# Kernel optimization log

Measured on AMD Instinct MI355X. Metric: run time of the kernel, lower is better.

The kernel has to match this reference:

```python
import jax, jax.numpy as jnp
import numpy as np

HIDDEN = 3072
NUM_HEADS = 24
HEAD_DIM = HIDDEN // NUM_HEADS  # 128
MLP_HIDDEN = 4 * HIDDEN         # 12288
SEQ = 2048


def setup_inputs() -> dict:
    key = jax.random.key(0)
    ks = jax.random.split(key, 12)
    s = 0.02
    return {
        "x": jax.random.normal(ks[0], (1, SEQ, HIDDEN), jnp.float32),
        "vec": jax.random.normal(ks[1], (1, HIDDEN), jnp.float32),
        "pe": jax.random.normal(ks[2], (1, 1, SEQ, HEAD_DIM // 2, 2, 2), jnp.float32),
        "mod_w": jax.random.normal(ks[3], (HIDDEN, 3 * HIDDEN), jnp.float32) * s,
        "mod_b": jnp.zeros((3 * HIDDEN,), jnp.float32),
        "lin1_w": jax.random.normal(ks[4], (HIDDEN, 3 * HIDDEN + MLP_HIDDEN), jnp.float32) * s,
        "lin1_b": jnp.zeros((3 * HIDDEN + MLP_HIDDEN,), jnp.float32),
        "lin2_w": jax.random.normal(ks[5], (HIDDEN + MLP_HIDDEN, HIDDEN), jnp.float32) * s,
        "lin2_b": jnp.zeros((HIDDEN,), jnp.float32),
        "q_scale": jnp.ones((HEAD_DIM,), jnp.float32),
        "k_scale": jnp.ones((HEAD_DIM,), jnp.float32),
    }


def _forward(x, vec, pe, mod_w, mod_b, lin1_w, lin1_b, lin2_w, lin2_b, q_scale, k_scale):
    B, L, H = x.shape
    NH, HD = NUM_HEADS, HEAD_DIM

    # Modulation: lin(silu(vec)) -> shift, scale, gate  (flux Modulation, double=False)
    mod = jnp.dot(jax.nn.silu(vec), mod_w) + mod_b          # (B, 3H)
    shift, scale, gate = jnp.split(mod, 3, axis=-1)
    shift, scale, gate = shift[:, None, :], scale[:, None, :], gate[:, None, :]

    # LayerNorm (no affine, eps=1e-6) + scale/shift modulation
    mu = jnp.mean(x, axis=-1, keepdims=True)
    var = jnp.mean((x - mu) ** 2, axis=-1, keepdims=True)
    xn = (x - mu) * jax.lax.rsqrt(var + 1e-6)
    x_mod = (1.0 + scale) * xn + shift

    # Fused QKV + MLP projection
    h = jnp.dot(x_mod, lin1_w) + lin1_b                     # (B, L, 3H + MLP)
    qkv, mlp = h[..., : 3 * H], h[..., 3 * H :]
    qkv = qkv.reshape(B, L, 3, NH, HD).transpose(2, 0, 3, 1, 4)  # (3, B, NH, L, HD)
    q, k, v = qkv[0], qkv[1], qkv[2]

    # QKNorm: RMSNorm over head_dim with learned scale (eps=1e-6)
    def rms(t, s):
        return t * jax.lax.rsqrt(jnp.mean(t * t, axis=-1, keepdims=True) + 1e-6) * s

    q = rms(q, q_scale)
    k = rms(k, k_scale)

    # Rotary embedding: pe is (B, 1, L, HD/2, 2, 2) of rotation matrix rows
    def rope(t):
        tr = t.reshape(B, NH, L, HD // 2, 1, 2)
        out = pe[..., 0] * tr[..., 0] + pe[..., 1] * tr[..., 1]  # (B, NH, L, HD/2, 2)
        return out.reshape(B, NH, L, HD)

    q, k = rope(q), rope(k)

    # Scaled dot-product attention (default 1/sqrt(HD) scale)
    scores = jnp.einsum("bhqd,bhkd->bhqk", q, k) / jnp.sqrt(jnp.float32(HD))
    attn = jnp.einsum("bhqk,bhkd->bhqd", jax.nn.softmax(scores, axis=-1), v)
    attn = attn.transpose(0, 2, 1, 3).reshape(B, L, H)

    # GELU(tanh) MLP branch, concat, output projection, gated residual
    mlp_act = jax.nn.gelu(mlp, approximate=True)
    out = jnp.dot(jnp.concatenate([attn, mlp_act], axis=-1), lin2_w) + lin2_b
    return x + gate * out


def reference(x, vec, pe, mod_w, mod_b, lin1_w, lin1_b, lin2_w, lin2_b, q_scale, k_scale):
    return _forward(x, vec, pe, mod_w, mod_b, lin1_w, lin1_b, lin2_w, lin2_b, q_scale, k_scale)
```

## Files before the change

kernel.cpp:

```cpp
#include <hip/hip_runtime.h>
#include <hip/hip_bf16.h>
#include <stdint.h>

#define SEQ   2048
#define HID   3072
#define NHEADS 24
#define HDIM  128
#define MLPD  12288
#define NCOL1 21504
#define NCOL2 15360
#define MOD3  9216
#define QKVW  9216
#define KSPLIT 8

typedef __attribute__((ext_vector_type(4))) float f32x4;
typedef __attribute__((ext_vector_type(8))) short bf16x8;
typedef __attribute__((ext_vector_type(4))) unsigned short u16x4;
typedef __attribute__((ext_vector_type(2))) unsigned short u16x2;

#define VMC(n) asm volatile("s_waitcnt vmcnt(" #n ")" ::: "memory")
#define SB()   __builtin_amdgcn_sched_barrier(0)

__device__ __forceinline__ unsigned short f2bf(float f){
  unsigned u = __float_as_uint(f);
  u = (u + 0x7fffu + ((u >> 16) & 1u)) >> 16;
  return (unsigned short)u;
}
__device__ __forceinline__ float bf2f(unsigned short u){
  return __uint_as_float(((unsigned)u) << 16);
}

__device__ __forceinline__ void gload_lds16(const void* g, void* l){
  __builtin_amdgcn_global_load_lds(
      (const __attribute__((address_space(1))) unsigned int*)g,
      (__attribute__((address_space(3))) unsigned int*)l, 16, 0, 0);
}

__device__ __forceinline__ float gelu_tanh(float x){
  float u = 0.7978845608028654f * (x + 0.044715f * x * x * x);
  float t = 1.f - 2.f / (__expf(2.f * u) + 1.f);
  return 0.5f * x * (1.f + t);
}

__global__ void silu_kernel(const float* __restrict__ vec, float* __restrict__ sv){
  int i = blockIdx.x * 256 + threadIdx.x;
  if (i < HID){ float v = vec[i]; sv[i] = v / (1.f + __expf(-v)); }
}

__global__ void mod_gemv(const float* __restrict__ sv, const float* __restrict__ W,
                         const float* __restrict__ b, float* __restrict__ mod){
  int n  = blockIdx.x * 32 + (threadIdx.x & 31);
  int ks = threadIdx.x >> 5;
  float acc = 0.f;
  int k0 = ks * 384;
  #pragma unroll 4
  for (int k = k0; k < k0 + 384; ++k)
    acc += sv[k] * W[(size_t)k * MOD3 + n];
  __shared__ float red[8][32];
  red[ks][threadIdx.x & 31] = acc;
  __syncthreads();
  if (ks == 0){
    float a = 0.f;
    #pragma unroll
    for (int i = 0; i < 8; ++i) a += red[i][threadIdx.x & 31];
    mod[n] = a + b[n];
  }
}

__global__ __launch_bounds__(256)
void ln_mod_kernel(const float* __restrict__ x, const float* __restrict__ mod,
                   unsigned short* __restrict__ xmod){
  int l = blockIdx.x, t = threadIdx.x;
  const float* row = x + (size_t)l * HID;
  f32x4 v[3];
  float s = 0.f, s2 = 0.f;
  #pragma unroll
  for (int i = 0; i < 3; ++i){
    v[i] = *(const f32x4*)(row + (t + i * 256) * 4);
    #pragma unroll
    for (int j = 0; j < 4; ++j){ s += v[i][j]; s2 += v[i][j] * v[i][j]; }
  }
  #pragma unroll
  for (int m = 1; m < 64; m <<= 1){ s += __shfl_xor(s, m, 64); s2 += __shfl_xor(s2, m, 64); }
  __shared__ float red[8];
  int wv = t >> 6, ln = t & 63;
  if (ln == 0){ red[wv] = s; red[4 + wv] = s2; }
  __syncthreads();
  s  = red[0] + red[1] + red[2] + red[3];
  s2 = red[4] + red[5] + red[6] + red[7];
  float mu  = s * (1.f / HID);
  float var = s2 * (1.f / HID) - mu * mu;
  float rs  = rsqrtf(var + 1e-6f);
  #pragma unroll
  for (int i = 0; i < 3; ++i){
    int c = (t + i * 256) * 4;
    f32x4 sh = *(const f32x4*)(mod + c);
    f32x4 sc = *(const f32x4*)(mod + HID + c);
    u16x4 o;
    #pragma unroll
    for (int j = 0; j < 4; ++j){
      float xn = (v[i][j] - mu) * rs;
      o[j] = f2bf((1.f + sc[j]) * xn + sh[j]);
    }
    *(u16x4*)(xmod + (size_t)l * HID + c) = o;
  }
}

__global__ __launch_bounds__(256)
void transpose_f2b(const float* __restrict__ in, unsigned short* __restrict__ out,
                   int R, int C){
  __shared__ float tile[64][65];
  int rt = blockIdx.y * 64, ct = blockIdx.x * 64;
  int t = threadIdx.x;
  int r0 = t >> 4, c0 = (t & 15) * 4;
  #pragma unroll
  for (int ph = 0; ph < 4; ++ph){
    int r = r0 + ph * 16;
    f32x4 v = *(const f32x4*)(in + (size_t)(rt + r) * C + ct + c0);
    tile[r][c0 + 0] = v[0]; tile[r][c0 + 1] = v[1];
    tile[r][c0 + 2] = v[2]; tile[r][c0 + 3] = v[3];
  }
  __syncthreads();
  #pragma unroll
  for (int ph = 0; ph < 4; ++ph){
    int r = r0 + ph * 16;
    u16x4 o;
    #pragma unroll
    for (int i = 0; i < 4; ++i) o[i] = f2bf(tile[c0 + i][r]);
    *(u16x4*)(out + (size_t)(ct + r) * R + rt + c0) = o;
  }
}

__global__ __launch_bounds__(256)
void transpose_b2b_head(const unsigned short* __restrict__ in,
                        unsigned short* __restrict__ out, int R, int C){
  __shared__ unsigned short tile[64][68];
  int h = blockIdx.z;
  const unsigned short* inh = in + (size_t)h * R * C;
  unsigned short* outh = out + (size_t)h * R * C;
  int rt = blockIdx.y * 64, ct = blockIdx.x * 64;
  int t = threadIdx.x;
  int r0 = t >> 4, c0 = (t & 15) * 4;
  #pragma unroll
  for (int ph = 0; ph < 4; ++ph){
    int r = r0 + ph * 16;
    u16x4 v = *(const u16x4*)(inh + (size_t)(rt + r) * C + ct + c0);
    tile[r][c0 + 0] = v[0]; tile[r][c0 + 1] = v[1];
    tile[r][c0 + 2] = v[2]; tile[r][c0 + 3] = v[3];
  }
  __syncthreads();
  #pragma unroll
  for (int ph = 0; ph < 4; ++ph){
    int r = r0 + ph * 16;
    u16x4 o;
    #pragma unroll
    for (int i = 0; i < 4; ++i) o[i] = tile[c0 + i][r];
    *(u16x4*)(outh + (size_t)(ct + r) * R + rt + c0) = o;
  }
}

__global__ void qkv_prep(const unsigned short* __restrict__ hq, const float* __restrict__ pe,
                         const float* __restrict__ qscale, const float* __restrict__ kscale,
                         unsigned short* __restrict__ qb, unsigned short* __restrict__ kb,
                         unsigned short* __restrict__ vb){
  int l = blockIdx.x, hh = blockIdx.y, lane = threadIdx.x;
  const unsigned short* row = hq + (size_t)l * QKVW;
  int d = lane * 2;
  u16x2 qv = *(const u16x2*)(row + hh * HDIM + d);
  u16x2 kv = *(const u16x2*)(row + HID + hh * HDIM + d);
  u16x2 vv = *(const u16x2*)(row + 2 * HID + hh * HDIM + d);
  float qx = bf2f(qv[0]), qy = bf2f(qv[1]);
  float kx = bf2f(kv[0]), ky = bf2f(kv[1]);
  float sq = qx * qx + qy * qy;
  float sk = kx * kx + ky * ky;
  #pragma unroll
  for (int m = 1; m < 64; m <<= 1){ sq += __shfl_xor(sq, m, 64); sk += __shfl_xor(sk, m, 64); }
  float rq = rsqrtf(sq * (1.f / HDIM) + 1e-6f);
  float rk = rsqrtf(sk * (1.f / HDIM) + 1e-6f);
  float2 qs2 = *(const float2*)(qscale + d);
  float2 ks2 = *(const float2*)(kscale + d);
  float q0 = qx * rq * qs2.x, q1 = qy * rq * qs2.y;
  float k0 = kx * rk * ks2.x, k1 = ky * rk * ks2.y;
  f32x4 p4 = *(const f32x4*)(pe + (size_t)l * 256 + lane * 4);
  const float sscl = 0.08838834764831845f;
  float qo0 = (p4[0] * q0 + p4[1] * q1) * sscl;
  float qo1 = (p4[2] * q0 + p4[3] * q1) * sscl;
  float ko0 =  p4[0] * k0 + p4[1] * k1;
  float ko1 =  p4[2] * k0 + p4[3] * k1;
  size_t base = ((size_t)hh * SEQ + l) * HDIM + d;
  u16x2 o;
  o[0] = f2bf(qo0); o[1] = f2bf(qo1); *(u16x2*)(qb + base) = o;
  o[0] = f2bf(ko0); o[1] = f2bf(ko1); *(u16x2*)(kb + base) = o;
  o[0] = vv[0];     o[1] = vv[1];     *(u16x2*)(vb + base) = o;
}

template<int EPI>
__global__ __launch_bounds__(512)
void gemm256(const unsigned short* __restrict__ A, const unsigned short* __restrict__ BT,
             const float* __restrict__ bias, unsigned short* __restrict__ out0,
             unsigned short* __restrict__ out1,
             int M, int N, int ldA, int ldB, int kchunk){
  __shared__ unsigned short Ls[65536];
  int nxy = gridDim.x * gridDim.y;
  int nwg = nxy * gridDim.z;
  int fid = (blockIdx.z * gridDim.y + blockIdx.y) * gridDim.x + blockIdx.x;
  int nid = (fid & 7) * (nwg >> 3) + (fid >> 3);
  int ksz = nid / nxy, rem = nid % nxy;
  int bm  = rem % gridDim.y, bn = rem / gridDim.y;
  int k0 = ksz * kchunk;
  int nk = kchunk >> 6;
  int tid = threadIdx.x, wave = tid >> 6, lane = tid & 63, lg = lane >> 4, lr = lane & 15;
  int wr = wave >> 2, wc = wave & 3;

  int G0 = tid, G1 = tid + 512;
  int r0 = G0 >> 2, r1 = G1 >> 2;
  int c0 = ((G0 & 3) ^ ((r0 >> 1) & 3)) * 8;
  int c1 = ((G1 & 3) ^ ((r1 >> 1) & 3)) * 8;
  const unsigned short* A0 = A  + (size_t)(bm * 256 + r0) * ldA + k0 + c0;
  const unsigned short* A1 = A  + (size_t)(bm * 256 + r1) * ldA + k0 + c1;
  const unsigned short* B0 = BT + (size_t)(bn * 256 + r0) * ldB + k0 + c0;
  const unsigned short* B1 = BT + (size_t)(bn * 256 + r1) * ldB + k0 + c1;
  unsigned short* LA = Ls;
  unsigned short* LB = Ls + 32768;
  int d0 = (wave * 64) * 8, d1 = (512 + wave * 64) * 8;

  auto stageA = [&](int t, int kh){
    unsigned short* h = LA + (((t & 1) * 2 + kh) << 13);
    int kc = t * 64 + kh * 32;
    gload_lds16(A0 + kc, h + d0);
    gload_lds16(A1 + kc, h + d1);
  };
  auto stageB = [&](int t, int kh){
    unsigned short* h = LB + (((t & 1) * 2 + kh) << 13);
    int kc = t * 64 + kh * 32;
    gload_lds16(B0 + kc, h + d0);
    gload_lds16(B1 + kc, h + d1);
  };

  int offA[8], offB[4];
  #pragma unroll
  for (int m = 0; m < 8; ++m){
    int row = wr * 128 + m * 16 + lr;
    offA[m] = row * 32 + ((lg ^ ((row >> 1) & 3)) * 8);
  }
  #pragma unroll
  for (int n = 0; n < 4; ++n){
    int row = wc * 64 + n * 16 + lr;
    offB[n] = row * 32 + ((lg ^ ((row >> 1) & 3)) * 8);
  }

  const f32x4 fz = 0.0f;
  f32x4 acc[8][4];
  #pragma unroll
  for (int i = 0; i < 8; ++i)
    #pragma unroll
    for (int j = 0; j < 4; ++j) acc[i][j] = fz;

  stageA(0, 0); stageB(0, 0); stageA(0, 1); stageB(0, 1); stageA(1, 0); stageB(1, 0);
  VMC(8);
  __builtin_amdgcn_s_barrier();
  SB();

  for (int t = 0; t < nk; ++t){
    const unsigned short* Ah = LA + (((t & 1) * 2) << 13);
    const unsigned short* Bh = LB + (((t & 1) * 2) << 13);
    bf16x8 fA[8], fB[4], gA[8], gB[4];
    #pragma unroll
    for (int m = 0; m < 4; ++m) fA[m] = *(const bf16x8*)&Ah[offA[m]];
    #pragma unroll
    for (int n = 0; n < 4; ++n) fB[n] = *(const bf16x8*)&Bh[offB[n]];
    #pragma unroll
    for (int m = 4; m < 8; ++m) fA[m] = *(const bf16x8*)&Ah[offA[m]];
    if (t + 1 < nk) stageA(t + 1, 1);
    SB();
    __builtin_amdgcn_s_barrier();
    SB();
    __builtin_amdgcn_s_setprio(1);
    #pragma unroll
    for (int m = 0; m < 4; ++m)
      #pragma unroll
      for (int n = 0; n < 4; ++n)
        acc[m][n] = __builtin_amdgcn_mfma_f32_16x16x32_bf16(fA[m], fB[n], acc[m][n], 0, 0, 0);
    __builtin_amdgcn_s_setprio(0);
    SB();
    __builtin_amdgcn_s_barrier();
    if (t + 1 < nk) stageB(t + 1, 1);
    SB();
    if (t == nk - 1) VMC(0);
    else             VMC(8);
    __builtin_amdgcn_s_barrier();
    SB();
    #pragma unroll
    for (int m = 0; m < 4; ++m) gA[m] = *(const bf16x8*)&Ah[8192 + offA[m]];
    #pragma unroll
    for (int n = 0; n < 4; ++n) gB[n] = *(const bf16x8*)&Bh[8192 + offB[n]];
    SB();
    __builtin_amdgcn_s_setprio(1);
    #pragma unroll
    for (int m = 0; m < 4; ++m)
      #pragma unroll
      for (int n = 0; n < 4; ++n)
        acc[m + 4][n] = __builtin_amdgcn_mfma_f32_16x16x32_bf16(fA[m + 4], fB[n], acc[m + 4][n], 0, 0, 0);
    __builtin_amdgcn_s_setprio(0);
    SB();
    __builtin_amdgcn_s_barrier();
    #pragma unroll
    for (int m = 4; m < 8; ++m) gA[m] = *(const bf16x8*)&Ah[8192 + offA[m]];
    if (t + 2 < nk) stageA(t + 2, 0);
    SB();
    __builtin_amdgcn_s_barrier();
    SB();
    __builtin_amdgcn_s_setprio(1);
    #pragma unroll
    for (int m = 0; m < 4; ++m)
      #pragma unroll
      for (int n = 0; n < 4; ++n)
        acc[m][n] = __builtin_amdgcn_mfma_f32_16x16x32_bf16(gA[m], gB[n], acc[m][n], 0, 0, 0);
    __builtin_amdgcn_s_setprio(0);
    SB();
    __builtin_amdgcn_s_barrier();
    if (t + 2 < nk) stageB(t + 2, 0);
    SB();
    if (t <= nk - 3)      VMC(8);
    else if (t == nk - 2) VMC(4);
    __builtin_amdgcn_s_barrier();
    SB();
    __builtin_amdgcn_s_setprio(1);
    #pragma unroll
    for (int m = 0; m < 4; ++m)
      #pragma unroll
      for (int n = 0; n < 4; ++n)
        acc[m + 4][n] = __builtin_amdgcn_mfma_f32_16x16x32_bf16(gA[m + 4], gB[n], acc[m + 4][n], 0, 0, 0);
    __builtin_amdgcn_s_setprio(0);
    SB();
    __builtin_amdgcn_s_barrier();
  }

  if constexpr (EPI == 0){
    if (bn < MOD3 / 256){
      #pragma unroll
      for (int m = 0; m < 8; ++m)
        #pragma unroll
        for (int n = 0; n < 4; ++n){
          int col = bn * 256 + wc * 64 + n * 16 + lr;
          float bv = bias[col];
          #pragma unroll
          for (int jj = 0; jj < 4; ++jj){
            int row = bm * 256 + wr * 128 + m * 16 + lg * 4 + jj;
            out0[(size_t)row * QKVW + col] = f2bf(acc[m][n][jj] + bv);
          }
        }
    } else {
      #pragma unroll
      for (int m = 0; m < 8; ++m)
        #pragma unroll
        for (int n = 0; n < 4; ++n){
          int col = bn * 256 + wc * 64 + n * 16 + lr;
          float bv = bias[col];
          #pragma unroll
          for (int jj = 0; jj < 4; ++jj){
            int row = bm * 256 + wr * 128 + m * 16 + lg * 4 + jj;
            out1[(size_t)row * NCOL2 + (col - 2 * HID)] = f2bf(gelu_tanh(acc[m][n][jj] + bv));
          }
        }
    }
  } else {
    unsigned short* P = out0 + (size_t)ksz * M * N;
    #pragma unroll
    for (int m = 0; m < 8; ++m)
      #pragma unroll
      for (int n = 0; n < 4; ++n){
        int col = bn * 256 + wc * 64 + n * 16 + lr;
        #pragma unroll
        for (int jj = 0; jj < 4; ++jj){
          int row = bm * 256 + wr * 128 + m * 16 + lg * 4 + jj;
          P[(size_t)row * N + col] = f2bf(acc[m][n][jj]);
        }
      }
  }
}

__global__ __launch_bounds__(256)
void reduce_lin2(const unsigned short* __restrict__ part, const float* __restrict__ x,
                 const float* __restrict__ gate, const float* __restrict__ bias,
                 float* __restrict__ out){
  int i4 = blockIdx.x * 256 + threadIdx.x;
  int c4 = i4 % (HID / 4);
  f32x4 s = 0.0f;
  #pragma unroll
  for (int ks = 0; ks < KSPLIT; ++ks){
    u16x4 p = *(const u16x4*)(part + (size_t)ks * SEQ * HID + (size_t)i4 * 4);
    #pragma unroll
    for (int j = 0; j < 4; ++j) s[j] += bf2f(p[j]);
  }
  f32x4 xv = *(const f32x4*)(x + (size_t)i4 * 4);
  f32x4 gv = *(const f32x4*)(gate + c4 * 4);
  f32x4 bv = *(const f32x4*)(bias + c4 * 4);
  f32x4 o;
  #pragma unroll
  for (int j = 0; j < 4; ++j) o[j] = xv[j] + gv[j] * (s[j] + bv[j]);
  *(f32x4*)(out + (size_t)i4 * 4) = o;
}

__global__ __launch_bounds__(256)
void attn_kernel(const unsigned short* __restrict__ qb, const unsigned short* __restrict__ kb,
                 const unsigned short* __restrict__ vt, unsigned short* __restrict__ a2){
  __shared__ unsigned short Ksm[64 * 128];
  __shared__ unsigned short Vsm[128 * 64];
  __shared__ unsigned short Psm[4][16 * 64];
  int fid = blockIdx.y * gridDim.x + blockIdx.x;
  int nid = (fid & 7) * 96 + (fid >> 3);
  int hh = nid / (SEQ / 64), qt = nid % (SEQ / 64);
  int tid = threadIdx.x, wave = tid >> 6, lane = tid & 63, lg = lane >> 4, lr = lane & 15;
  const unsigned short* Kh = kb + (size_t)hh * SEQ * HDIM;
  const unsigned short* Vh = vt + (size_t)hh * HDIM * SEQ;
  const unsigned short* Qh = qb + (size_t)hh * SEQ * HDIM;
  int q0 = qt * 64 + wave * 16;

  bf16x8 aq[4];
  #pragma unroll
  for (int kk = 0; kk < 4; ++kk)
    aq[kk] = *(const bf16x8*)(Qh + (size_t)(q0 + lr) * HDIM + kk * 32 + lg * 8);

  const f32x4 fzero = 0.0f;
  f32x4 acc_o[8];
  #pragma unroll
  for (int n = 0; n < 8; ++n) acc_o[n] = fzero;
  float mrun[4] = {-1e30f, -1e30f, -1e30f, -1e30f};
  float lrun[4] = {0.f, 0.f, 0.f, 0.f};

  for (int t = 0; t < SEQ / 64; ++t){
    __syncthreads();
    const unsigned short* Kt = Kh + (size_t)t * 64 * HDIM;
    const unsigned short* Vt = Vh + t * 64;
    #pragma unroll
    for (int r = 0; r < 4; ++r){
      int G  = r * 256 + tid;
      int Gs = G ^ ((G >> 4) & 7);
      gload_lds16(Kt + Gs * 8, (void*)&Ksm[(r * 256 + wave * 64) * 8]);
      int Gv = G ^ ((G >> 3) & 7);
      gload_lds16(Vt + (size_t)(Gv >> 3) * SEQ + (Gv & 7) * 8,
                  (void*)&Vsm[(r * 256 + wave * 64) * 8]);
    }
    __syncthreads();

    f32x4 sacc[4];
    #pragma unroll
    for (int j = 0; j < 4; ++j) sacc[j] = fzero;
    #pragma unroll
    for (int j = 0; j < 4; ++j){
      int kv = j * 16 + lr;
      #pragma unroll
      for (int kk = 0; kk < 4; ++kk){
        int bo = kv * 256 + (kk * 32 + lg * 8) * 2;
        bo ^= (kv & 7) << 4;
        bf16x8 bk = *(const bf16x8*)((const char*)Ksm + bo);
        sacc[j] = __builtin_amdgcn_mfma_f32_16x16x32_bf16(aq[kk], bk, sacc[j], 0, 0, 0);
      }
    }
    float scl[4], psum[4];
    #pragma unroll
    for (int jj = 0; jj < 4; ++jj){
      float m_ = fmaxf(fmaxf(sacc[0][jj], sacc[1][jj]), fmaxf(sacc[2][jj], sacc[3][jj]));
      #pragma unroll
      for (int mk = 1; mk < 16; mk <<= 1) m_ = fmaxf(m_, __shfl_xor(m_, mk, 64));
      float mn = fmaxf(mrun[jj], m_);
      scl[jj] = __expf(mrun[jj] - mn);
      mrun[jj] = mn;
      psum[jj] = 0.f;
    }
    #pragma unroll
    for (int j = 0; j < 4; ++j)
      #pragma unroll
      for (int jj = 0; jj < 4; ++jj){
        float p = __expf(sacc[j][jj] - mrun[jj]);
        sacc[j][jj] = p;
        psum[jj] += p;
      }
    #pragma unroll
    for (int jj = 0; jj < 4; ++jj){
      float ps = psum[jj];
      #pragma unroll
      for (int mk = 1; mk < 16; mk <<= 1) ps += __shfl_xor(ps, mk, 64);
      lrun[jj] = lrun[jj] * scl[jj] + ps;
    }
    #pragma unroll
    for (int n = 0; n < 8; ++n)
      #pragma unroll
      for (int jj = 0; jj < 4; ++jj) acc_o[n][jj] *= scl[jj];
    unsigned short* Pw = Psm[wave];
    #pragma unroll
    for (int j = 0; j < 4; ++j)
      #pragma unroll
      for (int jj = 0; jj < 4; ++jj){
        int prow = lg * 4 + jj, pcol = j * 16 + lr;
        int bo = prow * 128 + pcol * 2;
        bo ^= (prow & 7) << 4;
        *(unsigned short*)((char*)Pw + bo) = f2bf(sacc[j][jj]);
      }
    __syncthreads();
    #pragma unroll
    for (int k2 = 0; k2 < 2; ++k2){
      int bo = lr * 128 + (k2 * 32 + lg * 8) * 2;
      bo ^= (lr & 7) << 4;
      bf16x8 pf = *(const bf16x8*)((const char*)Pw + bo);
      #pragma unroll
      for (int n = 0; n < 8; ++n){
        int dd = n * 16 + lr;
        int vb_ = dd * 128 + (k2 * 32 + lg * 8) * 2;
        vb_ ^= (dd & 7) << 4;
        bf16x8 vf = *(const bf16x8*)((const char*)Vsm + vb_);
        acc_o[n] = __builtin_amdgcn_mfma_f32_16x16x32_bf16(pf, vf, acc_o[n], 0, 0, 0);
      }
    }
  }
  #pragma unroll
  for (int jj = 0; jj < 4; ++jj) lrun[jj] = 1.f / lrun[jj];
  #pragma unroll
  for (int n = 0; n < 8; ++n)
    #pragma unroll
    for (int jj = 0; jj < 4; ++jj){
      int row = q0 + lg * 4 + jj;
      int col = hh * HDIM + n * 16 + lr;
      a2[(size_t)row * NCOL2 + col] = f2bf(acc_o[n][jj] * lrun[jj]);
    }
}

extern "C" void kernel_launch(void* const* d_in, const int* in_sizes, int n_in,
                              void* d_out, int out_size, void* d_ws, size_t ws_size,
                              hipStream_t stream){
  const float* x       = (const float*)d_in[0];
  const float* vec     = (const float*)d_in[1];
  const float* pe      = (const float*)d_in[2];
  const float* mod_w   = (const float*)d_in[3];
  const float* mod_b   = (const float*)d_in[4];
  const float* lin1_w  = (const float*)d_in[5];
  const float* lin1_b  = (const float*)d_in[6];
  const float* lin2_w  = (const float*)d_in[7];
  const float* lin2_b  = (const float*)d_in[8];
  const float* q_scale = (const float*)d_in[9];
  const float* k_scale = (const float*)d_in[10];
  float* out = (float*)d_out;

  char* ws = (char*)d_ws;
  size_t off = 0;
  auto alloc = [&](size_t bytes){ void* p = ws + off; off += (bytes + 255) & ~(size_t)255; return p; };
  float* sv            = (float*)alloc((size_t)HID * 4);
  float* mod           = (float*)alloc((size_t)MOD3 * 4);
  unsigned short* xmod = (unsigned short*)alloc((size_t)SEQ * HID * 2);
  unsigned short* wt2  = (unsigned short*)alloc((size_t)HID * NCOL2 * 2);
  unsigned short* a2   = (unsigned short*)alloc((size_t)SEQ * NCOL2 * 2);
  unsigned short* qb   = (unsigned short*)alloc((size_t)NHEADS * SEQ * HDIM * 2);
  unsigned short* kb   = (unsigned short*)alloc((size_t)NHEADS * SEQ * HDIM * 2);
  unsigned short* vb   = (unsigned short*)alloc((size_t)NHEADS * SEQ * HDIM * 2);
  unsigned short* vt   = (unsigned short*)alloc((size_t)NHEADS * SEQ * HDIM * 2);
  unsigned short* wt1  = (unsigned short*)alloc((size_t)NCOL1 * HID * 2);
  unsigned short* hq   = (unsigned short*)alloc((size_t)SEQ * QKVW * 2);
  unsigned short* part = qb;

  silu_kernel<<<12, 256, 0, stream>>>(vec, sv);
  mod_gemv<<<MOD3 / 32, 256, 0, stream>>>(sv, mod_w, mod_b, mod);
  transpose_f2b<<<dim3(NCOL1 / 64, HID / 64), 256, 0, stream>>>(lin1_w, wt1, HID, NCOL1);
  transpose_f2b<<<dim3(HID / 64, NCOL2 / 64), 256, 0, stream>>>(lin2_w, wt2, NCOL2, HID);
  ln_mod_kernel<<<SEQ, 256, 0, stream>>>(x, mod, xmod);
  gemm256<0><<<dim3(NCOL1 / 256, SEQ / 256, 1), 512, 0, stream>>>(
      xmod, wt1, lin1_b, hq, a2, SEQ, NCOL1, HID, HID, HID);
  qkv_prep<<<dim3(SEQ, NHEADS), 64, 0, stream>>>(hq, pe, q_scale, k_scale, qb, kb, vb);
  transpose_b2b_head<<<dim3(HDIM / 64, SEQ / 64, NHEADS), 256, 0, stream>>>(vb, vt, SEQ, HDIM);
  attn_kernel<<<dim3(SEQ / 64, NHEADS), 256, 0, stream>>>(qb, kb, vt, a2);
  gemm256<2><<<dim3(HID / 256, SEQ / 256, KSPLIT), 512, 0, stream>>>(
      a2, wt2, nullptr, part, nullptr, SEQ, HID, NCOL2, NCOL2, NCOL2 / KSPLIT);
  reduce_lin2<<<SEQ * HID / 4 / 256, 256, 0, stream>>>(part, x, mod + 2 * HID, lin2_b, out);
}
```

Baseline: 834.7 us.

## Double-buffer K/V tiles in attention and fuse SiLU into modulation GEMV

Attention now keeps two LDS buffers for K and V and prefetches the next tile with async global-to-LDS loads while computing the current one, synchronized by vmcnt waits and raw barriers. The barrier after writing P is replaced by a per-wave LDS wait, since each wave only reads its own P. Separately, the SiLU of the modulation vector is computed inline in the GEMV, removing a kernel launch and a workspace buffer. The extra LDS doubles K/V shared memory usage, which may reduce occupancy.

```diff
diff --git a/kernel.cpp b/kernel.cpp
--- a/kernel.cpp
+++ b/kernel.cpp
@@ -42,20 +42,18 @@
   return 0.5f * x * (1.f + t);
 }
 
-__global__ void silu_kernel(const float* __restrict__ vec, float* __restrict__ sv){
-  int i = blockIdx.x * 256 + threadIdx.x;
-  if (i < HID){ float v = vec[i]; sv[i] = v / (1.f + __expf(-v)); }
-}
-
-__global__ void mod_gemv(const float* __restrict__ sv, const float* __restrict__ W,
+__global__ void mod_gemv(const float* __restrict__ vec, const float* __restrict__ W,
                          const float* __restrict__ b, float* __restrict__ mod){
   int n  = blockIdx.x * 32 + (threadIdx.x & 31);
   int ks = threadIdx.x >> 5;
   float acc = 0.f;
   int k0 = ks * 384;
   #pragma unroll 4
-  for (int k = k0; k < k0 + 384; ++k)
-    acc += sv[k] * W[(size_t)k * MOD3 + n];
+  for (int k = k0; k < k0 + 384; ++k){
+    float v = vec[k];
+    float s = v / (1.f + __expf(-v));
+    acc += s * W[(size_t)k * MOD3 + n];
+  }
   __shared__ float red[8][32];
   red[ks][threadIdx.x & 31] = acc;
   __syncthreads();
@@ -405,8 +403,8 @@
 __global__ __launch_bounds__(256)
 void attn_kernel(const unsigned short* __restrict__ qb, const unsigned short* __restrict__ kb,
                  const unsigned short* __restrict__ vt, unsigned short* __restrict__ a2){
-  __shared__ unsigned short Ksm[64 * 128];
-  __shared__ unsigned short Vsm[128 * 64];
+  __shared__ unsigned short Ksm[2][64 * 128];
+  __shared__ unsigned short Vsm[2][128 * 64];
   __shared__ unsigned short Psm[4][16 * 64];
   int fid = blockIdx.y * gridDim.x + blockIdx.x;
   int nid = (fid & 7) * 96 + (fid >> 3);
@@ -429,20 +427,28 @@
   float mrun[4] = {-1e30f, -1e30f, -1e30f, -1e30f};
   float lrun[4] = {0.f, 0.f, 0.f, 0.f};
 
-  for (int t = 0; t < SEQ / 64; ++t){
-    __syncthreads();
+  auto stage = [&](int t){
+    int buf = t & 1;
     const unsigned short* Kt = Kh + (size_t)t * 64 * HDIM;
     const unsigned short* Vt = Vh + t * 64;
     #pragma unroll
     for (int r = 0; r < 4; ++r){
       int G  = r * 256 + tid;
       int Gs = G ^ ((G >> 4) & 7);
-      gload_lds16(Kt + Gs * 8, (void*)&Ksm[(r * 256 + wave * 64) * 8]);
+      gload_lds16(Kt + Gs * 8, (void*)&Ksm[buf][(r * 256 + wave * 64) * 8]);
       int Gv = G ^ ((G >> 3) & 7);
       gload_lds16(Vt + (size_t)(Gv >> 3) * SEQ + (Gv & 7) * 8,
-                  (void*)&Vsm[(r * 256 + wave * 64) * 8]);
-    }
-    __syncthreads();
+                  (void*)&Vsm[buf][(r * 256 + wave * 64) * 8]);
+    }
+  };
+
+  stage(0);
+  for (int t = 0; t < SEQ / 64; ++t){
+    int buf = t & 1;
+    if (t + 1 < SEQ / 64){ stage(t + 1); VMC(8); }
+    else                 { VMC(0); }
+    __builtin_amdgcn_s_barrier();
+    SB();
 
     f32x4 sacc[4];
     #pragma unroll
@@ -454,7 +460,7 @@
       for (int kk = 0; kk < 4; ++kk){
         int bo = kv * 256 + (kk * 32 + lg * 8) * 2;
         bo ^= (kv & 7) << 4;
-        bf16x8 bk = *(const bf16x8*)((const char*)Ksm + bo);
+        bf16x8 bk = *(const bf16x8*)((const char*)Ksm[buf] + bo);
         sacc[j] = __builtin_amdgcn_mfma_f32_16x16x32_bf16(aq[kk], bk, sacc[j], 0, 0, 0);
       }
     }
@@ -498,7 +504,8 @@
         bo ^= (prow & 7) << 4;
         *(unsigned short*)((char*)Pw + bo) = f2bf(sacc[j][jj]);
       }
-    __syncthreads();
+    asm volatile("s_waitcnt lgkmcnt(0)" ::: "memory");
+    SB();
     #pragma unroll
     for (int k2 = 0; k2 < 2; ++k2){
       int bo = lr * 128 + (k2 * 32 + lg * 8) * 2;
@@ -509,10 +516,12 @@
         int dd = n * 16 + lr;
         int vb_ = dd * 128 + (k2 * 32 + lg * 8) * 2;
         vb_ ^= (dd & 7) << 4;
-        bf16x8 vf = *(const bf16x8*)((const char*)Vsm + vb_);
+        bf16x8 vf = *(const bf16x8*)((const char*)Vsm[buf] + vb_);
         acc_o[n] = __builtin_amdgcn_mfma_f32_16x16x32_bf16(pf, vf, acc_o[n], 0, 0, 0);
       }
     }
+    SB();
+    __builtin_amdgcn_s_barrier();
   }
   #pragma unroll
   for (int jj = 0; jj < 4; ++jj) lrun[jj] = 1.f / lrun[jj];
@@ -545,7 +554,6 @@
   char* ws = (char*)d_ws;
   size_t off = 0;
   auto alloc = [&](size_t bytes){ void* p = ws + off; off += (bytes + 255) & ~(size_t)255; return p; };
-  float* sv            = (float*)alloc((size_t)HID * 4);
   float* mod           = (float*)alloc((size_t)MOD3 * 4);
   unsigned short* xmod = (unsigned short*)alloc((size_t)SEQ * HID * 2);
   unsigned short* wt2  = (unsigned short*)alloc((size_t)HID * NCOL2 * 2);
@@ -558,8 +566,7 @@
   unsigned short* hq   = (unsigned short*)alloc((size_t)SEQ * QKVW * 2);
   unsigned short* part = qb;
 
-  silu_kernel<<<12, 256, 0, stream>>>(vec, sv);
-  mod_gemv<<<MOD3 / 32, 256, 0, stream>>>(sv, mod_w, mod_b, mod);
+  mod_gemv<<<MOD3 / 32, 256, 0, stream>>>(vec, mod_w, mod_b, mod);
   transpose_f2b<<<dim3(NCOL1 / 64, HID / 64), 256, 0, stream>>>(lin1_w, wt1, HID, NCOL1);
   transpose_f2b<<<dim3(HID / 64, NCOL2 / 64), 256, 0, stream>>>(lin2_w, wt2, NCOL2, HID);
   ln_mod_kernel<<<SEQ, 256, 0, stream>>>(x, mod, xmod);
```

New measurement: 841.8 us. About the same (+0.9%).

## Restructure GEMM staging into row-halves with full-K64 tiles and new wave mapping

Applied to the files above, without the earlier changes.

The 256x256 GEMM main loop now stages LDS by row halves (rows 0-127 and 128-255), each holding the full 64-wide K slice with an 8-way XOR swizzle, instead of splitting K into two 32-wide halves. Each wave now owns four 64x32 quadrant sub-tiles. It loads A and B fragments once per K step and reuses them across two K sub-steps, which cuts LDS reads and barriers per iteration. Wait counts and the epilogue row/column mapping are rewritten to match. This risks higher register pressure and subtle sync or waitcnt mistakes at the pipeline edges.

```diff
diff --git a/kernel.cpp b/kernel.cpp
--- a/kernel.cpp
+++ b/kernel.cpp
@@ -212,41 +212,41 @@
   int tid = threadIdx.x, wave = tid >> 6, lane = tid & 63, lg = lane >> 4, lr = lane & 15;
   int wr = wave >> 2, wc = wave & 3;
 
-  int G0 = tid, G1 = tid + 512;
-  int r0 = G0 >> 2, r1 = G1 >> 2;
-  int c0 = ((G0 & 3) ^ ((r0 >> 1) & 3)) * 8;
-  int c1 = ((G1 & 3) ^ ((r1 >> 1) & 3)) * 8;
-  const unsigned short* A0 = A  + (size_t)(bm * 256 + r0) * ldA + k0 + c0;
-  const unsigned short* A1 = A  + (size_t)(bm * 256 + r1) * ldA + k0 + c1;
-  const unsigned short* B0 = BT + (size_t)(bn * 256 + r0) * ldB + k0 + c0;
-  const unsigned short* B1 = BT + (size_t)(bn * 256 + r1) * ldB + k0 + c1;
-  unsigned short* LA = Ls;
-  unsigned short* LB = Ls + 32768;
+  int rh = tid >> 3;
+  int sc = (((tid & 7) ^ (rh & 7)) * 8);
+  const unsigned short* pA0 = A  + (size_t)(bm * 256 + rh     ) * ldA + k0 + sc;
+  const unsigned short* pA1 = A  + (size_t)(bm * 256 + rh + 64) * ldA + k0 + sc;
+  const unsigned short* pB0 = BT + (size_t)(bn * 256 + rh     ) * ldB + k0 + sc;
+  const unsigned short* pB1 = BT + (size_t)(bn * 256 + rh + 64) * ldB + k0 + sc;
   int d0 = (wave * 64) * 8, d1 = (512 + wave * 64) * 8;
 
-  auto stageA = [&](int t, int kh){
-    unsigned short* h = LA + (((t & 1) * 2 + kh) << 13);
-    int kc = t * 64 + kh * 32;
-    gload_lds16(A0 + kc, h + d0);
-    gload_lds16(A1 + kc, h + d1);
+  auto stageA = [&](int t, int half){
+    unsigned short* h = Ls + (((t & 1) * 2 + half) << 13);
+    size_t ro = (size_t)(half * 128) * ldA + t * 64;
+    gload_lds16(pA0 + ro, h + d0);
+    gload_lds16(pA1 + ro, h + d1);
   };
-  auto stageB = [&](int t, int kh){
-    unsigned short* h = LB + (((t & 1) * 2 + kh) << 13);
-    int kc = t * 64 + kh * 32;
-    gload_lds16(B0 + kc, h + d0);
-    gload_lds16(B1 + kc, h + d1);
+  auto stageB = [&](int t, int half){
+    unsigned short* h = Ls + 32768 + (((t & 1) * 2 + half) << 13);
+    size_t ro = (size_t)(half * 128) * ldB + t * 64;
+    gload_lds16(pB0 + ro, h + d0);
+    gload_lds16(pB1 + ro, h + d1);
   };
 
-  int offA[8], offB[4];
-  #pragma unroll
-  for (int m = 0; m < 8; ++m){
-    int row = wr * 128 + m * 16 + lr;
-    offA[m] = row * 32 + ((lg ^ ((row >> 1) & 3)) * 8);
-  }
-  #pragma unroll
-  for (int n = 0; n < 4; ++n){
-    int row = wc * 64 + n * 16 + lr;
-    offB[n] = row * 32 + ((lg ^ ((row >> 1) & 3)) * 8);
+  int offA[4][2], offB[2][2];
+  #pragma unroll
+  for (int mm = 0; mm < 4; ++mm){
+    int row = wr * 64 + mm * 16 + lr;
+    #pragma unroll
+    for (int ks = 0; ks < 2; ++ks)
+      offA[mm][ks] = row * 64 + (((ks * 4 + lg) ^ (row & 7)) * 8);
+  }
+  #pragma unroll
+  for (int nn = 0; nn < 2; ++nn){
+    int row = wc * 32 + nn * 16 + lr;
+    #pragma unroll
+    for (int ks = 0; ks < 2; ++ks)
+      offB[nn][ks] = row * 64 + (((ks * 4 + lg) ^ (row & 7)) * 8);
   }
 
   const f32x4 fz = 0.0f;
@@ -256,84 +256,91 @@
     #pragma unroll
     for (int j = 0; j < 4; ++j) acc[i][j] = fz;
 
-  stageA(0, 0); stageB(0, 0); stageA(0, 1); stageB(0, 1); stageA(1, 0); stageB(1, 0);
-  VMC(8);
-  __builtin_amdgcn_s_barrier();
-  SB();
+  stageA(0, 0); stageB(0, 0); stageB(0, 1); stageA(0, 1);
+  if (nk > 1){ stageA(1, 0); stageB(1, 0); }
 
   for (int t = 0; t < nk; ++t){
-    const unsigned short* Ah = LA + (((t & 1) * 2) << 13);
-    const unsigned short* Bh = LB + (((t & 1) * 2) << 13);
-    bf16x8 fA[8], fB[4], gA[8], gB[4];
-    #pragma unroll
-    for (int m = 0; m < 4; ++m) fA[m] = *(const bf16x8*)&Ah[offA[m]];
-    #pragma unroll
-    for (int n = 0; n < 4; ++n) fB[n] = *(const bf16x8*)&Bh[offB[n]];
-    #pragma unroll
-    for (int m = 4; m < 8; ++m) fA[m] = *(const bf16x8*)&Ah[offA[m]];
-    if (t + 1 < nk) stageA(t + 1, 1);
-    SB();
+    const unsigned short* Au_ = Ls + (((t & 1) * 2 + 0) << 13);
+    const unsigned short* Al_ = Ls + (((t & 1) * 2 + 1) << 13);
+    const unsigned short* Bu_ = Ls + 32768 + (((t & 1) * 2 + 0) << 13);
+    const unsigned short* Bl_ = Ls + 32768 + (((t & 1) * 2 + 1) << 13);
+    bool more1 = (t + 1 < nk), more2 = (t + 2 < nk);
+    bf16x8 am[4][2], am4[4][2], b01[2][2], b23[2][2];
+    if (more1) VMC(8); else VMC(4);
     __builtin_amdgcn_s_barrier();
     SB();
+    #pragma unroll
+    for (int mm = 0; mm < 4; ++mm)
+      #pragma unroll
+      for (int ks = 0; ks < 2; ++ks) am[mm][ks] = *(const bf16x8*)&Au_[offA[mm][ks]];
+    #pragma unroll
+    for (int nn = 0; nn < 2; ++nn)
+      #pragma unroll
+      for (int ks = 0; ks < 2; ++ks) b01[nn][ks] = *(const bf16x8*)&Bu_[offB[nn][ks]];
+    if (more1) stageB(t + 1, 1);
+    SB();
     __builtin_amdgcn_s_setprio(1);
     #pragma unroll
-    for (int m = 0; m < 4; ++m)
-      #pragma unroll
-      for (int n = 0; n < 4; ++n)
-        acc[m][n] = __builtin_amdgcn_mfma_f32_16x16x32_bf16(fA[m], fB[n], acc[m][n], 0, 0, 0);
+    for (int mm = 0; mm < 4; ++mm)
+      #pragma unroll
+      for (int nn = 0; nn < 2; ++nn)
+        #pragma unroll
+        for (int ks = 0; ks < 2; ++ks)
+          acc[mm][nn] = __builtin_amdgcn_mfma_f32_16x16x32_bf16(am[mm][ks], b01[nn][ks], acc[mm][nn], 0, 0, 0);
     __builtin_amdgcn_s_setprio(0);
     SB();
+    if (more1) VMC(8); else VMC(2);
     __builtin_amdgcn_s_barrier();
-    if (t + 1 < nk) stageB(t + 1, 1);
-    SB();
-    if (t == nk - 1) VMC(0);
-    else             VMC(8);
+    SB();
+    #pragma unroll
+    for (int nn = 0; nn < 2; ++nn)
+      #pragma unroll
+      for (int ks = 0; ks < 2; ++ks) b23[nn][ks] = *(const bf16x8*)&Bl_[offB[nn][ks]];
+    if (more1) stageA(t + 1, 1);
+    SB();
+    __builtin_amdgcn_s_setprio(1);
+    #pragma unroll
+    for (int mm = 0; mm < 4; ++mm)
+      #pragma unroll
+      for (int nn = 0; nn < 2; ++nn)
+        #pragma unroll
+        for (int ks = 0; ks < 2; ++ks)
+          acc[mm][nn + 2] = __builtin_amdgcn_mfma_f32_16x16x32_bf16(am[mm][ks], b23[nn][ks], acc[mm][nn + 2], 0, 0, 0);
+    __builtin_amdgcn_s_setprio(0);
+    SB();
+    if (more1) VMC(8); else VMC(0);
     __builtin_amdgcn_s_barrier();
     SB();
     #pragma unroll
-    for (int m = 0; m < 4; ++m) gA[m] = *(const bf16x8*)&Ah[8192 + offA[m]];
-    #pragma unroll
-    for (int n = 0; n < 4; ++n) gB[n] = *(const bf16x8*)&Bh[8192 + offB[n]];
+    for (int mm = 0; mm < 4; ++mm)
+      #pragma unroll
+      for (int ks = 0; ks < 2; ++ks) am4[mm][ks] = *(const bf16x8*)&Al_[offA[mm][ks]];
+    if (more2) stageA(t + 2, 0);
     SB();
     __builtin_amdgcn_s_setprio(1);
     #pragma unroll
-    for (int m = 0; m < 4; ++m)
-      #pragma unroll
-      for (int n = 0; n < 4; ++n)
-        acc[m + 4][n] = __builtin_amdgcn_mfma_f32_16x16x32_bf16(fA[m + 4], fB[n], acc[m + 4][n], 0, 0, 0);
+    for (int mm = 0; mm < 4; ++mm)
+      #pragma unroll
+      for (int nn = 0; nn < 2; ++nn)
+        #pragma unroll
+        for (int ks = 0; ks < 2; ++ks)
+          acc[mm + 4][nn] = __builtin_amdgcn_mfma_f32_16x16x32_bf16(am4[mm][ks], b01[nn][ks], acc[mm + 4][nn], 0, 0, 0);
     __builtin_amdgcn_s_setprio(0);
     SB();
     __builtin_amdgcn_s_barrier();
-    #pragma unroll
-    for (int m = 4; m < 8; ++m) gA[m] = *(const bf16x8*)&Ah[8192 + offA[m]];
-    if (t + 2 < nk) stageA(t + 2, 0);
-    SB();
-    __builtin_amdgcn_s_barrier();
+    SB();
+    if (more2) stageB(t + 2, 0);
     SB();
     __builtin_amdgcn_s_setprio(1);
     #pragma unroll
-    for (int m = 0; m < 4; ++m)
-      #pragma unroll
-      for (int n = 0; n < 4; ++n)
-        acc[m][n] = __builtin_amdgcn_mfma_f32_16x16x32_bf16(gA[m], gB[n], acc[m][n], 0, 0, 0);
+    for (int mm = 0; mm < 4; ++mm)
+      #pragma unroll
+      for (int nn = 0; nn < 2; ++nn)
+        #pragma unroll
+        for (int ks = 0; ks < 2; ++ks)
+          acc[mm + 4][nn + 2] = __builtin_amdgcn_mfma_f32_16x16x32_bf16(am4[mm][ks], b23[nn][ks], acc[mm + 4][nn + 2], 0, 0, 0);
     __builtin_amdgcn_s_setprio(0);
     SB();
-    __builtin_amdgcn_s_barrier();
-    if (t + 2 < nk) stageB(t + 2, 0);
-    SB();
-    if (t <= nk - 3)      VMC(8);
-    else if (t == nk - 2) VMC(4);
-    __builtin_amdgcn_s_barrier();
-    SB();
-    __builtin_amdgcn_s_setprio(1);
-    #pragma unroll
-    for (int m = 0; m < 4; ++m)
-      #pragma unroll
-      for (int n = 0; n < 4; ++n)
-        acc[m + 4][n] = __builtin_amdgcn_mfma_f32_16x16x32_bf16(gA[m + 4], gB[n], acc[m + 4][n], 0, 0, 0);
-    __builtin_amdgcn_s_setprio(0);
-    SB();
-    __builtin_amdgcn_s_barrier();
   }
 
   if constexpr (EPI == 0){
@@ -342,11 +349,11 @@
       for (int m = 0; m < 8; ++m)
         #pragma unroll
         for (int n = 0; n < 4; ++n){
-          int col = bn * 256 + wc * 64 + n * 16 + lr;
+          int col = bn * 256 + wc * 32 + (n & 1) * 16 + (n >> 1) * 128 + lr;
           float bv = bias[col];
           #pragma unroll
           for (int jj = 0; jj < 4; ++jj){
-            int row = bm * 256 + wr * 128 + m * 16 + lg * 4 + jj;
+            int row = bm * 256 + wr * 64 + (m & 3) * 16 + (m >> 2) * 128 + lg * 4 + jj;
             out0[(size_t)row * QKVW + col] = f2bf(acc[m][n][jj] + bv);
           }
         }
@@ -355,11 +362,11 @@
       for (int m = 0; m < 8; ++m)
         #pragma unroll
         for (int n = 0; n < 4; ++n){
-          int col = bn * 256 + wc * 64 + n * 16 + lr;
+          int col = bn * 256 + wc * 32 + (n & 1) * 16 + (n >> 1) * 128 + lr;
           float bv = bias[col];
           #pragma unroll
           for (int jj = 0; jj < 4; ++jj){
-            int row = bm * 256 + wr * 128 + m * 16 + lg * 4 + jj;
+            int row = bm * 256 + wr * 64 + (m & 3) * 16 + (m >> 2) * 128 + lg * 4 + jj;
             out1[(size_t)row * NCOL2 + (col - 2 * HID)] = f2bf(gelu_tanh(acc[m][n][jj] + bv));
           }
         }
@@ -370,10 +377,10 @@
     for (int m = 0; m < 8; ++m)
       #pragma unroll
       for (int n = 0; n < 4; ++n){
-        int col = bn * 256 + wc * 64 + n * 16 + lr;
+        int col = bn * 256 + wc * 32 + (n & 1) * 16 + (n >> 1) * 128 + lr;
         #pragma unroll
         for (int jj = 0; jj < 4; ++jj){
-          int row = bm * 256 + wr * 128 + m * 16 + lg * 4 + jj;
+          int row = bm * 256 + wr * 64 + (m & 3) * 16 + (m >> 2) * 128 + lg * 4 + jj;
           P[(size_t)row * N + col] = f2bf(acc[m][n][jj]);
         }
       }
```

Result: faster. 806.4 us (-3.4%).
